# Kernel optimization log

Hardware: AMD Instinct MI355X
Metric: run time of the kernel (lower is better)

Reference implementation:

```python
import jax, jax.numpy as jnp
import numpy as np

N_CLASSES = 4
N_FEATURES = 13
N_HIDDEN = 13
N_STEPS = 100
FORGET_BIAS = 1.0


def setup_inputs() -> dict:
    key = jax.random.key(0)
    ks = jax.random.split(key, 10)
    B = 32768
    return {
        "x_input": jax.random.normal(ks[0], (B, N_STEPS, N_FEATURES), dtype=jnp.float32),
        # input projection (tf.random.normal mean=0.5 in original; values irrelevant for correctness test)
        "w_hidden": jax.random.normal(ks[1], (N_FEATURES, N_HIDDEN), dtype=jnp.float32) * 0.5 + 0.5,
        "b_hidden": jax.random.normal(ks[2], (N_HIDDEN,), dtype=jnp.float32) * 0.5 + 0.5,
        # BasicLSTMCell params: kernel [input_dim + hidden, 4*hidden], gate order (i, j, f, o)
        "lstm0_kernel": jax.random.normal(ks[3], (N_HIDDEN + N_HIDDEN, 4 * N_HIDDEN), dtype=jnp.float32) * 0.2,
        "lstm0_bias": jnp.zeros((4 * N_HIDDEN,), dtype=jnp.float32),
        "lstm1_kernel": jax.random.normal(ks[4], (N_HIDDEN + N_HIDDEN, 4 * N_HIDDEN), dtype=jnp.float32) * 0.2,
        "lstm1_bias": jnp.zeros((4 * N_HIDDEN,), dtype=jnp.float32),
        "w_output": jax.random.normal(ks[5], (N_HIDDEN, N_CLASSES), dtype=jnp.float32) * 0.5 + 0.5,
        "b_output": jax.random.normal(ks[6], (N_CLASSES,), dtype=jnp.float32) * 0.5 + 0.5,
    }


def _lstm_cell(x, c, h, kernel, bias):
    # BasicLSTMCell: z = [x; h] @ W + b, split -> i, j, f, o
    z = jnp.concatenate([x, h], axis=-1) @ kernel + bias
    i, j, f, o = jnp.split(z, 4, axis=-1)
    c_new = c * jax.nn.sigmoid(f + FORGET_BIAS) + jax.nn.sigmoid(i) * jnp.tanh(j)
    h_new = jnp.tanh(c_new) * jax.nn.sigmoid(o)
    return c_new, h_new


def reference(x_input, w_hidden, b_hidden, lstm0_kernel, lstm0_bias,
              lstm1_kernel, lstm1_bias, w_output, b_output):
    B = x_input.shape[0]
    # input projection + relu, batched over all timesteps: [B,T,F] -> [T,B,H]
    hidden = jax.nn.relu(jnp.einsum('btf,fh->bth', x_input, w_hidden) + b_hidden)
    hidden = jnp.transpose(hidden, (1, 0, 2))  # [T, B, H]

    zeros = jnp.zeros((B, N_HIDDEN), dtype=x_input.dtype)
    init = (zeros, zeros, zeros, zeros)  # (c0, h0, c1, h1)

    def step(carry, x_t):
        c0, h0, c1, h1 = carry
        c0, h0 = _lstm_cell(x_t, c0, h0, lstm0_kernel, lstm0_bias)
        c1, h1 = _lstm_cell(h0, c1, h1, lstm1_kernel, lstm1_bias)
        return (c0, h0, c1, h1), None

    (c0, h0, c1, h1), _ = jax.lax.scan(step, init, hidden)
    # last output of top LSTM layer -> output projection
    return h1 @ w_output + b_output
```

## Files before the change

kernel.cpp:

```cpp
#include <hip/hip_runtime.h>
#include <cstdint>

typedef __bf16          bf16x8 __attribute__((ext_vector_type(8)));
typedef float           f32x4  __attribute__((ext_vector_type(4)));
typedef unsigned short  u16x8  __attribute__((ext_vector_type(8)));

#define MFMA16(a, b, c) __builtin_amdgcn_mfma_f32_16x16x32_bf16((a), (b), (c), 0, 0, 0)

__device__ __forceinline__ float fsig(float x) {
    float e = __builtin_amdgcn_exp2f(-1.4426950408889634f * x);
    return __builtin_amdgcn_rcpf(1.0f + e);
}
__device__ __forceinline__ float ftanh(float x) {
    float e = __builtin_amdgcn_exp2f(-2.8853900817779268f * x);
    return fmaf(2.0f, __builtin_amdgcn_rcpf(1.0f + e), -1.0f);
}
__device__ __forceinline__ void split2(float v, unsigned short& hi, unsigned short& lo) {
    unsigned u = __builtin_bit_cast(unsigned, v);
    hi = (unsigned short)(u >> 16);
    float rem = v - __builtin_bit_cast(float, u & 0xffff0000u);
    lo = (unsigned short)(__builtin_bit_cast(unsigned, rem) >> 16);
}


__global__ __launch_bounds__(256, 4)
void lstm_fused(const float* __restrict__ x,
                const float* __restrict__ w_hidden,
                const float* __restrict__ b_hidden,
                const float* __restrict__ k0,
                const float* __restrict__ b0,
                const float* __restrict__ k1,
                const float* __restrict__ b1,
                const float* __restrict__ w_out,
                const float* __restrict__ b_out,
                float* __restrict__ out)
{
    __shared__ __attribute__((aligned(16))) unsigned short xh_s[2][2][2][384];
    __shared__ __attribute__((aligned(16))) unsigned short h0_s[2][2][2][384];
    __shared__ __attribute__((aligned(16))) unsigned short h1_s[2][2][384];

    const int lane = threadIdx.x & 63;
    const int wv   = threadIdx.x >> 6;
    const int grp  = wv >> 1;
    const int role = wv & 1;
    const int col  = lane & 15;
    const int q    = lane >> 4;
    const int qh   = q & 1;
    const int s0   = (blockIdx.x * 2 + grp) * 16;

    for (int i = threadIdx.x; i < 2 * 2 * 2 * 384; i += 256) ((unsigned short*)h0_s)[i] = 0;
    for (int i = threadIdx.x; i < 2 * 2 * 384;     i += 256) ((unsigned short*)h1_s)[i] = 0;

    const float* kp = role ? k1 : k0;
    const float* bb = role ? b1 : b0;
    bf16x8 Kh[4], Kl[4];
    #pragma unroll
    for (int g = 0; g < 4; ++g) {
        bf16x8 hv{}, lv{};
        #pragma unroll
        for (int j = 0; j < 8; ++j) {
            int k = 8 * q + j;
            float w = 0.f;
            if (col < 13) {
                int rr = -1;
                if (k < 13) rr = k;
                else if (k >= 16 && k < 29) rr = 13 + (k - 16);
                if (rr >= 0) w = kp[rr * 52 + 13 * g + col];
            }
            unsigned short h_, l_;
            split2(w, h_, l_);
            hv[j] = __builtin_bit_cast(__bf16, h_);
            lv[j] = __builtin_bit_cast(__bf16, l_);
        }
        Kh[g] = hv; Kl[g] = lv;
    }
    const float bi  = (col < 13) ? bb[col]      : 0.f;
    const float bj  = (col < 13) ? bb[13 + col] : 0.f;
    const float bf_ = (col < 13) ? bb[26 + col] : 0.f;
    const float bo_ = (col < 13) ? bb[39 + col] : 0.f;

    bf16x8 Ph{}, Pl{}, Oh{}, Ol{};
    float bp = 0.f, bob = 0.f;
    if (role) {
        #pragma unroll
        for (int j = 0; j < 8; ++j) {
            int k = 8 * q + j;
            float wp = (k < 13 && col < 13) ? w_hidden[k * 13 + col] : 0.f;
            float wo = (k < 13 && col < 4)  ? w_out[k * 4 + col]     : 0.f;
            unsigned short h_, l_;
            split2(wp, h_, l_); Ph[j] = __builtin_bit_cast(__bf16, h_); Pl[j] = __builtin_bit_cast(__bf16, l_);
            split2(wo, h_, l_); Oh[j] = __builtin_bit_cast(__bf16, h_); Ol[j] = __builtin_bit_cast(__bf16, l_);
        }
        bp  = (col < 13) ? b_hidden[col] : 0.f;
        bob = (col < 4)  ? b_out[col]    : 0.f;
    }

    const float* xrow = x + (size_t)(s0 + col) * 1300;
    const int ro = 4 * q * 24 + col;

    auto do_proj = [&](int t, unsigned short* oH, unsigned short* oL) {
        const float* p = xrow + t * 13;
        float xv[8];
        #pragma unroll
        for (int j = 0; j < 8; ++j) xv[j] = 0.f;
        if (q == 0) {
            #pragma unroll
            for (int j = 0; j < 8; ++j) xv[j] = p[j];
        } else if (q == 1) {
            #pragma unroll
            for (int j = 0; j < 5; ++j) xv[j] = p[8 + j];
        }
        bf16x8 axh, axl;
        #pragma unroll
        for (int j = 0; j < 8; ++j) {
            unsigned short h_, l_;
            split2(xv[j], h_, l_);
            axh[j] = __builtin_bit_cast(__bf16, h_);
            axl[j] = __builtin_bit_cast(__bf16, l_);
        }
        f32x4 zp = {bp, bp, bp, bp};
        zp = MFMA16(axh, Ph, zp);
        zp = MFMA16(axl, Ph, zp);
        zp = MFMA16(axh, Pl, zp);
        #pragma unroll
        for (int r = 0; r < 4; ++r) {
            float v = fmaxf(zp[r], 0.f);
            unsigned short hh, hl;
            split2(v, hh, hl);
            oH[ro + r * 24] = hh;
            oL[ro + r * 24] = hl;
        }
    };

    auto do_cell = [&](const unsigned short* inH, const unsigned short* inL,
                       const unsigned short* hidH, const unsigned short* hidL,
                       f32x4& cst, unsigned short* oH, unsigned short* oL) {
        const unsigned short* pH = (q < 2) ? inH : hidH;
        const unsigned short* pL = (q < 2) ? inL : hidL;
        bf16x8 ah = __builtin_bit_cast(bf16x8, *(const u16x8*)(pH + col * 24 + 8 * qh));
        bf16x8 al = __builtin_bit_cast(bf16x8, *(const u16x8*)(pL + col * 24 + 8 * qh));
        f32x4 zi = {bi, bi, bi, bi};
        f32x4 zj = {bj, bj, bj, bj};
        f32x4 zf = {bf_, bf_, bf_, bf_};
        f32x4 zo = {bo_, bo_, bo_, bo_};
        zi = MFMA16(ah, Kh[0], zi); zi = MFMA16(al, Kh[0], zi); zi = MFMA16(ah, Kl[0], zi);
        zj = MFMA16(ah, Kh[1], zj); zj = MFMA16(al, Kh[1], zj); zj = MFMA16(ah, Kl[1], zj);
        zf = MFMA16(ah, Kh[2], zf); zf = MFMA16(al, Kh[2], zf); zf = MFMA16(ah, Kl[2], zf);
        zo = MFMA16(ah, Kh[3], zo); zo = MFMA16(al, Kh[3], zo); zo = MFMA16(ah, Kl[3], zo);
        #pragma unroll
        for (int r = 0; r < 4; ++r) {
            float si = fsig(zi[r]);
            float tj = ftanh(zj[r]);
            float sf = fsig(zf[r] + 1.0f);
            float so = fsig(zo[r]);
            float cn = fmaf(cst[r], sf, si * tj);
            cst[r] = cn;
            float hv = ftanh(cn) * so;
            unsigned short hh, hl;
            split2(hv, hh, hl);
            oH[ro + r * 24] = hh;
            oL[ro + r * 24] = hl;
        }
    };

    f32x4 cst = {0.f, 0.f, 0.f, 0.f};

    if (role) do_proj(0, &xh_s[grp][0][0][0], &xh_s[grp][0][1][0]);
    __syncthreads();

    for (int i = 0; i <= 100; ++i) {
        if (role == 0) {
            if (i < 100) {
                int rb = i & 1, pb = (i + 1) & 1;
                do_cell(&xh_s[grp][rb][0][0], &xh_s[grp][rb][1][0],
                        &h0_s[grp][pb][0][0], &h0_s[grp][pb][1][0],
                        cst,
                        &h0_s[grp][rb][0][0], &h0_s[grp][rb][1][0]);
            }
        } else {
            if (i >= 1) {
                int rb = (i - 1) & 1;
                do_cell(&h0_s[grp][rb][0][0], &h0_s[grp][rb][1][0],
                        &h1_s[grp][0][0], &h1_s[grp][1][0],
                        cst,
                        &h1_s[grp][0][0], &h1_s[grp][1][0]);
            }
            if (i < 99) {
                int tb = (i + 1) & 1;
                do_proj(i + 1, &xh_s[grp][tb][0][0], &xh_s[grp][tb][1][0]);
            }
        }
        __syncthreads();
    }

    if (role) {
        const unsigned short* pH = &h1_s[grp][0][0];
        const unsigned short* pL = &h1_s[grp][1][0];
        bf16x8 afh = __builtin_bit_cast(bf16x8, *(const u16x8*)(pH + col * 24 + 8 * qh));
        bf16x8 afl = __builtin_bit_cast(bf16x8, *(const u16x8*)(pL + col * 24 + 8 * qh));
        f32x4 zfin = {bob, bob, bob, bob};
        zfin = MFMA16(afh, Oh, zfin);
        zfin = MFMA16(afl, Oh, zfin);
        zfin = MFMA16(afh, Ol, zfin);
        if (col < 4) {
            #pragma unroll
            for (int r = 0; r < 4; ++r)
                out[(size_t)(s0 + 4 * q + r) * 4 + col] = zfin[r];
        }
    }
}

extern "C" void kernel_launch(void* const* d_in, const int* in_sizes, int n_in,
                              void* d_out, int out_size, void* d_ws, size_t ws_size,
                              hipStream_t stream) {
    (void)in_sizes; (void)n_in; (void)d_ws; (void)ws_size; (void)out_size;
    lstm_fused<<<dim3(1024), dim3(256), 0, stream>>>(
        (const float*)d_in[0], (const float*)d_in[1], (const float*)d_in[2],
        (const float*)d_in[3], (const float*)d_in[4], (const float*)d_in[5],
        (const float*)d_in[6], (const float*)d_in[7], (const float*)d_in[8],
        (float*)d_out);
}
```

Baseline: 380.6 us.

## Split LSTM gate work across main and helper waves with fused bias and merged sigmoid math

Moves from 2 to 4 waves per group: each layer gets a main wave doing the MFMAs and 3 of 4 output rows, and a helper wave that handles the 4th row via an LDS transfer and also runs the input projection. Biases are folded into the weight matrix through a constant-one input column, and the gate nonlinearities are rewritten to share reciprocals. h1 is now double-buffered. The aim is to shorten the serial per-step critical path, at the cost of an extra barrier per step and a larger block that may lower occupancy.

```diff
diff --git a/kernel.cpp b/kernel.cpp
--- a/kernel.cpp
+++ b/kernel.cpp
@@ -5,25 +5,23 @@
 typedef float           f32x4  __attribute__((ext_vector_type(4)));
 typedef unsigned short  u16x8  __attribute__((ext_vector_type(8)));
 
-#define MFMA16(a, b, c) __builtin_amdgcn_mfma_f32_16x16x32_bf16((a), (b), (c), 0, 0, 0)
-
-__device__ __forceinline__ float fsig(float x) {
-    float e = __builtin_amdgcn_exp2f(-1.4426950408889634f * x);
-    return __builtin_amdgcn_rcpf(1.0f + e);
-}
-__device__ __forceinline__ float ftanh(float x) {
-    float e = __builtin_amdgcn_exp2f(-2.8853900817779268f * x);
-    return fmaf(2.0f, __builtin_amdgcn_rcpf(1.0f + e), -1.0f);
-}
+#define MFMA16(a,b,c) __builtin_amdgcn_mfma_f32_16x16x32_bf16((a),(b),(c),0,0,0)
+
+__device__ __forceinline__ float rcpf(float x) { return __builtin_amdgcn_rcpf(x); }
+__device__ __forceinline__ float ex2(float x)  { return __builtin_amdgcn_exp2f(x); }
+
 __device__ __forceinline__ void split2(float v, unsigned short& hi, unsigned short& lo) {
     unsigned u = __builtin_bit_cast(unsigned, v);
     hi = (unsigned short)(u >> 16);
     float rem = v - __builtin_bit_cast(float, u & 0xffff0000u);
     lo = (unsigned short)(__builtin_bit_cast(unsigned, rem) >> 16);
 }
-
-
-__global__ __launch_bounds__(256, 4)
+__device__ __forceinline__ __bf16 bfbits(unsigned short b) { return __builtin_bit_cast(__bf16, b); }
+
+
+constexpr float KL = 1.4426950408889634f;
+
+__global__ __launch_bounds__(512, 8)
 void lstm_fused(const float* __restrict__ x,
                 const float* __restrict__ w_hidden,
                 const float* __restrict__ b_hidden,
@@ -37,175 +35,205 @@
 {
     __shared__ __attribute__((aligned(16))) unsigned short xh_s[2][2][2][384];
     __shared__ __attribute__((aligned(16))) unsigned short h0_s[2][2][2][384];
-    __shared__ __attribute__((aligned(16))) unsigned short h1_s[2][2][384];
-
-    const int lane = threadIdx.x & 63;
-    const int wv   = threadIdx.x >> 6;
-    const int grp  = wv >> 1;
-    const int role = wv & 1;
-    const int col  = lane & 15;
-    const int q    = lane >> 4;
-    const int qh   = q & 1;
-    const int s0   = (blockIdx.x * 2 + grp) * 16;
-
-    for (int i = threadIdx.x; i < 2 * 2 * 2 * 384; i += 256) ((unsigned short*)h0_s)[i] = 0;
-    for (int i = threadIdx.x; i < 2 * 2 * 384;     i += 256) ((unsigned short*)h1_s)[i] = 0;
-
-    const float* kp = role ? k1 : k0;
-    const float* bb = role ? b1 : b0;
+    __shared__ __attribute__((aligned(16))) unsigned short h1_s[2][2][2][384];
+    __shared__ __attribute__((aligned(16))) f32x4 xfer[2][2][64];
+
+    const int lane   = threadIdx.x & 63;
+    const int wv     = threadIdx.x >> 6;
+    const int grp    = wv >> 2;
+    const int role   = wv & 3;
+    const int layer  = role >> 1;
+    const int helper = role & 1;
+    const int col    = lane & 15;
+    const int q      = lane >> 4;
+    const int qh     = q & 1;
+    const int s0     = (blockIdx.x * 2 + grp) * 16;
+
+    {
+        unsigned short* a0 = &xh_s[0][0][0][0];
+        unsigned short* a1 = &h0_s[0][0][0][0];
+        unsigned short* a2 = &h1_s[0][0][0][0];
+        for (int idx = threadIdx.x; idx < 3072; idx += 512) {
+            unsigned short v = ((idx % 24) == 13 && ((idx / 384) & 1) == 0) ? (unsigned short)0x3F80 : (unsigned short)0;
+            a0[idx] = v; a1[idx] = v; a2[idx] = v;
+        }
+    }
+
     bf16x8 Kh[4], Kl[4];
-    #pragma unroll
-    for (int g = 0; g < 4; ++g) {
+    if (!helper) {
+        const float* kp = layer ? k1 : k0;
+        const float* bb = layer ? b1 : b0;
+        #pragma unroll
+        for (int g = 0; g < 4; ++g) {
+            bf16x8 hv{}, lv{};
+            #pragma unroll
+            for (int j = 0; j < 8; ++j) {
+                int k = 8 * q + j;
+                float w = 0.f;
+                if (col < 13) {
+                    if (k < 13)                 w = kp[k * 52 + 13 * g + col];
+                    else if (k == 13)           w = bb[13 * g + col] + (g == 2 ? 1.f : 0.f);
+                    else if (k >= 16 && k < 29) w = kp[(13 + k - 16) * 52 + 13 * g + col];
+                }
+                unsigned short h_, l_;
+                split2(w, h_, l_);
+                hv[j] = bfbits(h_); lv[j] = bfbits(l_);
+            }
+            Kh[g] = hv; Kl[g] = lv;
+        }
+    } else {
         bf16x8 hv{}, lv{};
         #pragma unroll
         for (int j = 0; j < 8; ++j) {
             int k = 8 * q + j;
             float w = 0.f;
             if (col < 13) {
-                int rr = -1;
-                if (k < 13) rr = k;
-                else if (k >= 16 && k < 29) rr = 13 + (k - 16);
-                if (rr >= 0) w = kp[rr * 52 + 13 * g + col];
+                if (k < 13)       w = w_hidden[k * 13 + col];
+                else if (k == 13) w = b_hidden[col];
             }
             unsigned short h_, l_;
             split2(w, h_, l_);
-            hv[j] = __builtin_bit_cast(__bf16, h_);
-            lv[j] = __builtin_bit_cast(__bf16, l_);
-        }
-        Kh[g] = hv; Kl[g] = lv;
-    }
-    const float bi  = (col < 13) ? bb[col]      : 0.f;
-    const float bj  = (col < 13) ? bb[13 + col] : 0.f;
-    const float bf_ = (col < 13) ? bb[26 + col] : 0.f;
-    const float bo_ = (col < 13) ? bb[39 + col] : 0.f;
-
-    bf16x8 Ph{}, Pl{}, Oh{}, Ol{};
-    float bp = 0.f, bob = 0.f;
-    if (role) {
-        #pragma unroll
-        for (int j = 0; j < 8; ++j) {
-            int k = 8 * q + j;
-            float wp = (k < 13 && col < 13) ? w_hidden[k * 13 + col] : 0.f;
-            float wo = (k < 13 && col < 4)  ? w_out[k * 4 + col]     : 0.f;
-            unsigned short h_, l_;
-            split2(wp, h_, l_); Ph[j] = __builtin_bit_cast(__bf16, h_); Pl[j] = __builtin_bit_cast(__bf16, l_);
-            split2(wo, h_, l_); Oh[j] = __builtin_bit_cast(__bf16, h_); Ol[j] = __builtin_bit_cast(__bf16, l_);
-        }
-        bp  = (col < 13) ? b_hidden[col] : 0.f;
-        bob = (col < 4)  ? b_out[col]    : 0.f;
+            hv[j] = bfbits(h_); lv[j] = bfbits(l_);
+        }
+        Kh[0] = hv; Kh[1] = lv;
     }
 
     const float* xrow = x + (size_t)(s0 + col) * 1300;
-    const int ro = 4 * q * 24 + col;
-
-    auto do_proj = [&](int t, unsigned short* oH, unsigned short* oL) {
-        const float* p = xrow + t * 13;
-        float xv[8];
-        #pragma unroll
-        for (int j = 0; j < 8; ++j) xv[j] = 0.f;
-        if (q == 0) {
+    float cst0 = 0.f, cst1 = 0.f, cst2 = 0.f;
+
+    auto elem = [&](float zi, float zj, float zf, float zo, float& c) -> float {
+        float a   = ex2(-KL * zi);
+        float b   = ex2(-2.f * KL * zj);
+        float fe  = ex2(-KL * zf);
+        float g   = ex2(-KL * zo);
+        float opa = 1.f + a, opb = 1.f + b, opf = 1.f + fe;
+        float pab = opa * opb;
+        float r1  = rcpf(pab * opf);
+        float cn  = fmaf(c, pab, (1.f - b) * opf) * r1;
+        c = cn;
+        float d   = ex2(-2.f * KL * cn);
+        float r2  = rcpf((1.f + d) * (1.f + g));
+        return (1.f - d) * r2;
+    };
+
+    auto cell_main = [&](const unsigned short* inH, const unsigned short* hidH,
+                         unsigned short* outH) {
+        const unsigned short* pA = (q < 2) ? inH : hidH;
+        bf16x8 ah = __builtin_bit_cast(bf16x8, *(const u16x8*)(pA + col * 24 + 8 * qh));
+        bf16x8 al = __builtin_bit_cast(bf16x8, *(const u16x8*)(pA + 384 + col * 24 + 8 * qh));
+        f32x4 z0 = {0.f,0.f,0.f,0.f}, z1 = z0, z2 = z0, z3 = z0;
+        z0 = MFMA16(ah, Kh[0], z0); z0 = MFMA16(al, Kh[0], z0); z0 = MFMA16(ah, Kl[0], z0);
+        z1 = MFMA16(ah, Kh[1], z1); z1 = MFMA16(al, Kh[1], z1); z1 = MFMA16(ah, Kl[1], z1);
+        z2 = MFMA16(ah, Kh[2], z2); z2 = MFMA16(al, Kh[2], z2); z2 = MFMA16(ah, Kl[2], z2);
+        z3 = MFMA16(ah, Kh[3], z3); z3 = MFMA16(al, Kh[3], z3); z3 = MFMA16(ah, Kl[3], z3);
+        xfer[grp][layer][lane] = (f32x4){z0[3], z1[3], z2[3], z3[3]};
+        float* cs[3] = {&cst0, &cst1, &cst2};
+        #pragma unroll
+        for (int r = 0; r < 3; ++r) {
+            float hv = elem(z0[r], z1[r], z2[r], z3[r], *cs[r]);
+            unsigned short hh, hl;
+            split2(hv, hh, hl);
+            if (col < 13) {
+                outH[(4 * q + r) * 24 + col]       = hh;
+                outH[384 + (4 * q + r) * 24 + col] = hl;
+            }
+        }
+    };
+
+    auto cell_help = [&](unsigned short* outH) {
+        f32x4 z = xfer[grp][layer][lane];
+        float hv = elem(z[0], z[1], z[2], z[3], cst0);
+        unsigned short hh, hl;
+        split2(hv, hh, hl);
+        if (col < 13) {
+            outH[(4 * q + 3) * 24 + col]       = hh;
+            outH[384 + (4 * q + 3) * 24 + col] = hl;
+        }
+    };
+
+    auto proj = [&](int t, unsigned short* oH) {
+        bf16x8 axh{}, axl{};
+        if (q < 2) {
+            const float* p = xrow + t * 13;
             #pragma unroll
-            for (int j = 0; j < 8; ++j) xv[j] = p[j];
-        } else if (q == 1) {
-            #pragma unroll
-            for (int j = 0; j < 5; ++j) xv[j] = p[8 + j];
-        }
-        bf16x8 axh, axl;
-        #pragma unroll
-        for (int j = 0; j < 8; ++j) {
-            unsigned short h_, l_;
-            split2(xv[j], h_, l_);
-            axh[j] = __builtin_bit_cast(__bf16, h_);
-            axl[j] = __builtin_bit_cast(__bf16, l_);
-        }
-        f32x4 zp = {bp, bp, bp, bp};
-        zp = MFMA16(axh, Ph, zp);
-        zp = MFMA16(axl, Ph, zp);
-        zp = MFMA16(axh, Pl, zp);
-        #pragma unroll
-        for (int r = 0; r < 4; ++r) {
+            for (int j = 0; j < 8; ++j) {
+                int k  = 8 * q + j;
+                int kk = k > 12 ? 12 : k;
+                float v = p[kk];
+                if (k > 12) v = 0.f;
+                unsigned short h_, l_;
+                split2(v, h_, l_);
+                axh[j] = bfbits(h_); axl[j] = bfbits(l_);
+            }
+            if (q == 1) { axh[5] = bfbits(0x3F80); axl[5] = bfbits(0); }
+        }
+        f32x4 zp = {0.f,0.f,0.f,0.f};
+        zp = MFMA16(axh, Kh[0], zp);
+        zp = MFMA16(axl, Kh[0], zp);
+        zp = MFMA16(axh, Kh[1], zp);
+        #pragma unroll
+        for (int rr = 0; rr < 2; ++rr) {
+            int r = 2 * layer + rr;
             float v = fmaxf(zp[r], 0.f);
             unsigned short hh, hl;
             split2(v, hh, hl);
-            oH[ro + r * 24] = hh;
-            oL[ro + r * 24] = hl;
-        }
-    };
-
-    auto do_cell = [&](const unsigned short* inH, const unsigned short* inL,
-                       const unsigned short* hidH, const unsigned short* hidL,
-                       f32x4& cst, unsigned short* oH, unsigned short* oL) {
-        const unsigned short* pH = (q < 2) ? inH : hidH;
-        const unsigned short* pL = (q < 2) ? inL : hidL;
-        bf16x8 ah = __builtin_bit_cast(bf16x8, *(const u16x8*)(pH + col * 24 + 8 * qh));
-        bf16x8 al = __builtin_bit_cast(bf16x8, *(const u16x8*)(pL + col * 24 + 8 * qh));
-        f32x4 zi = {bi, bi, bi, bi};
-        f32x4 zj = {bj, bj, bj, bj};
-        f32x4 zf = {bf_, bf_, bf_, bf_};
-        f32x4 zo = {bo_, bo_, bo_, bo_};
-        zi = MFMA16(ah, Kh[0], zi); zi = MFMA16(al, Kh[0], zi); zi = MFMA16(ah, Kl[0], zi);
-        zj = MFMA16(ah, Kh[1], zj); zj = MFMA16(al, Kh[1], zj); zj = MFMA16(ah, Kl[1], zj);
-        zf = MFMA16(ah, Kh[2], zf); zf = MFMA16(al, Kh[2], zf); zf = MFMA16(ah, Kl[2], zf);
-        zo = MFMA16(ah, Kh[3], zo); zo = MFMA16(al, Kh[3], zo); zo = MFMA16(ah, Kl[3], zo);
-        #pragma unroll
-        for (int r = 0; r < 4; ++r) {
-            float si = fsig(zi[r]);
-            float tj = ftanh(zj[r]);
-            float sf = fsig(zf[r] + 1.0f);
-            float so = fsig(zo[r]);
-            float cn = fmaf(cst[r], sf, si * tj);
-            cst[r] = cn;
-            float hv = ftanh(cn) * so;
-            unsigned short hh, hl;
-            split2(hv, hh, hl);
-            oH[ro + r * 24] = hh;
-            oL[ro + r * 24] = hl;
-        }
-    };
-
-    f32x4 cst = {0.f, 0.f, 0.f, 0.f};
-
-    if (role) do_proj(0, &xh_s[grp][0][0][0], &xh_s[grp][0][1][0]);
+            if (col < 13) {
+                oH[(4 * q + r) * 24 + col]       = hh;
+                oH[384 + (4 * q + r) * 24 + col] = hl;
+            }
+        }
+    };
+
     __syncthreads();
+    if (helper) proj(0, &xh_s[grp][0][0][0]);
+    __syncthreads();
 
     for (int i = 0; i <= 100; ++i) {
-        if (role == 0) {
-            if (i < 100) {
-                int rb = i & 1, pb = (i + 1) & 1;
-                do_cell(&xh_s[grp][rb][0][0], &xh_s[grp][rb][1][0],
-                        &h0_s[grp][pb][0][0], &h0_s[grp][pb][1][0],
-                        cst,
-                        &h0_s[grp][rb][0][0], &h0_s[grp][rb][1][0]);
+        int p = i & 1;
+        if (!helper) {
+            if (layer == 0) {
+                if (i < 100)
+                    cell_main(&xh_s[grp][p][0][0], &h0_s[grp][p ^ 1][0][0], &h0_s[grp][p][0][0]);
+            } else {
+                if (i >= 1)
+                    cell_main(&h0_s[grp][p ^ 1][0][0], &h1_s[grp][p][0][0], &h1_s[grp][p ^ 1][0][0]);
             }
         } else {
-            if (i >= 1) {
-                int rb = (i - 1) & 1;
-                do_cell(&h0_s[grp][rb][0][0], &h0_s[grp][rb][1][0],
-                        &h1_s[grp][0][0], &h1_s[grp][1][0],
-                        cst,
-                        &h1_s[grp][0][0], &h1_s[grp][1][0]);
-            }
-            if (i < 99) {
-                int tb = (i + 1) & 1;
-                do_proj(i + 1, &xh_s[grp][tb][0][0], &xh_s[grp][tb][1][0]);
-            }
+            if (i < 99) proj(i + 1, &xh_s[grp][p ^ 1][0][0]);
         }
         __syncthreads();
-    }
-
-    if (role) {
-        const unsigned short* pH = &h1_s[grp][0][0];
-        const unsigned short* pL = &h1_s[grp][1][0];
-        bf16x8 afh = __builtin_bit_cast(bf16x8, *(const u16x8*)(pH + col * 24 + 8 * qh));
-        bf16x8 afl = __builtin_bit_cast(bf16x8, *(const u16x8*)(pL + col * 24 + 8 * qh));
-        f32x4 zfin = {bob, bob, bob, bob};
-        zfin = MFMA16(afh, Oh, zfin);
-        zfin = MFMA16(afl, Oh, zfin);
-        zfin = MFMA16(afh, Ol, zfin);
+        if (helper) {
+            if (layer == 0) { if (i < 100) cell_help(&h0_s[grp][p][0][0]); }
+            else            { if (i >= 1)  cell_help(&h1_s[grp][p ^ 1][0][0]); }
+        }
+        __syncthreads();
+    }
+
+    if (helper && layer == 1) {
+        bf16x8 Oh{}, Ol{};
+        #pragma unroll
+        for (int j = 0; j < 8; ++j) {
+            int k = 8 * q + j;
+            float w = 0.f;
+            if (col < 4) {
+                if (k < 13)       w = w_out[k * 4 + col];
+                else if (k == 13) w = b_out[col];
+            }
+            unsigned short h_, l_;
+            split2(w, h_, l_);
+            Oh[j] = bfbits(h_); Ol[j] = bfbits(l_);
+        }
+        const unsigned short* pA = &h1_s[grp][1][0][0];
+        bf16x8 ah = __builtin_bit_cast(bf16x8, *(const u16x8*)(pA + col * 24 + 8 * qh));
+        bf16x8 al = __builtin_bit_cast(bf16x8, *(const u16x8*)(pA + 384 + col * 24 + 8 * qh));
+        f32x4 zf = {0.f,0.f,0.f,0.f};
+        zf = MFMA16(ah, Oh, zf);
+        zf = MFMA16(al, Oh, zf);
+        zf = MFMA16(ah, Ol, zf);
         if (col < 4) {
             #pragma unroll
             for (int r = 0; r < 4; ++r)
-                out[(size_t)(s0 + 4 * q + r) * 4 + col] = zfin[r];
+                out[(size_t)(s0 + 4 * q + r) * 4 + col] = zf[r];
         }
     }
 }
@@ -214,7 +242,7 @@
                               void* d_out, int out_size, void* d_ws, size_t ws_size,
                               hipStream_t stream) {
     (void)in_sizes; (void)n_in; (void)d_ws; (void)ws_size; (void)out_size;
-    lstm_fused<<<dim3(1024), dim3(256), 0, stream>>>(
+    lstm_fused<<<dim3(1024), dim3(512), 0, stream>>>(
         (const float*)d_in[0], (const float*)d_in[1], (const float*)d_in[2],
         (const float*)d_in[3], (const float*)d_in[4], (const float*)d_in[5],
         (const float*)d_in[6], (const float*)d_in[7], (const float*)d_in[8],
```

Result: slower. 576.1 us (+51.4%).
